# Optimization experiments

Hardware: AMD Instinct MI355X
Metric: run time of the kernel (lower is better)

## Reference

```python
import jax, jax.numpy as jnp
import numpy as np

NUM_SEGMENTS = 100000  # number of cycle slots (max cycle id + 1)


def setup_inputs() -> dict:
    key = jax.random.key(0)
    k1, k2, k3 = jax.random.split(key, 3)
    x = jax.random.randint(k1, (100000,), 0, 22, dtype=jnp.int64)
    atom_to_cycle = jax.random.randint(k2, (2, 600000), 0, NUM_SEGMENTS, dtype=jnp.int64)
    emb_weight = jax.random.normal(k3, (22, 128), dtype=jnp.float32)  # Embedding(22, hidden_dim)
    return {"x": x, "atom_to_cycle": atom_to_cycle, "emb_weight": emb_weight}


def reference(x, atom_to_cycle, emb_weight):
    # x: [N] int atom codes; atom_to_cycle: [2, E]; emb_weight: [22, D]
    h = emb_weight[x]                       # [N, D] embedding lookup
    gathered = h[atom_to_cycle[0]]          # [E, D] gather by atom index
    # scatter_sum over cycle ids -> [NUM_SEGMENTS, D]
    out = jax.ops.segment_sum(gathered, atom_to_cycle[1], num_segments=NUM_SEGMENTS)
    return out
```

## Files before the change

### kernel.cpp

```cpp
#include <hip/hip_runtime.h>
#include <stdint.h>

#define KCODES 22
#define KW     12

typedef int   int2v   __attribute__((ext_vector_type(2)));
typedef int   int4v   __attribute__((ext_vector_type(4)));
typedef float float4v __attribute__((ext_vector_type(4)));

#define BSHIFT   7
#define BROWS    128
#define BCAP     4096
#define EPT      8
#define CHUNK    2048
#define MAXBUCK  1024
#define GPAD     16

__global__ __launch_bounds__(256) void bin_edges(
        const int* __restrict__ a2c, const int* __restrict__ x,
        uint32_t* __restrict__ gcur, uint16_t* __restrict__ bins,
        int E, int nbuck) {
    __shared__ uint32_t lcnt[MAXBUCK];
    __shared__ uint32_t lbase[MAXBUCK];
    const int tid = threadIdx.x;
    for (int b = tid; b < nbuck; b += 256) lcnt[b] = 0;
    __syncthreads();

    const int base = blockIdx.x * CHUNK + tid * EPT;
    int atoms[EPT] __attribute__((aligned(16)));
    int cycs[EPT]  __attribute__((aligned(16)));
    if (((E & 3) == 0) && (base + EPT <= E)) {
        *(int4v*)(atoms + 0) = __builtin_nontemporal_load((const int4v*)(a2c + base));
        *(int4v*)(atoms + 4) = __builtin_nontemporal_load((const int4v*)(a2c + base) + 1);
        *(int4v*)(cycs + 0)  = __builtin_nontemporal_load((const int4v*)(a2c + E + base));
        *(int4v*)(cycs + 4)  = __builtin_nontemporal_load((const int4v*)(a2c + E + base) + 1);
    } else {
#pragma unroll
        for (int j = 0; j < EPT; ++j) {
            int e = base + j;
            atoms[j] = (e < E) ? a2c[e] : 0;
            cycs[j]  = (e < E) ? a2c[E + e] : -1;
        }
    }

    uint16_t val[EPT], bk[EPT], rk[EPT];
#pragma unroll
    for (int j = 0; j < EPT; ++j) {
        if (cycs[j] >= 0) {
            uint32_t code = (uint32_t)x[atoms[j]];
            uint32_t b    = (uint32_t)cycs[j] >> BSHIFT;
            bk[j]  = (uint16_t)b;
            rk[j]  = (uint16_t)atomicAdd(&lcnt[b], 1u);
            val[j] = (uint16_t)((((uint32_t)cycs[j] & (BROWS - 1)) << 5) | code);
        } else {
            bk[j] = 0xFFFFu;
        }
    }
    __syncthreads();

    for (int b = tid; b < nbuck; b += 256) {
        uint32_t c = lcnt[b];
        lbase[b] = c ? atomicAdd(&gcur[(size_t)b * GPAD], c) : 0u;
    }
    __syncthreads();

#pragma unroll
    for (int j = 0; j < EPT; ++j) {
        if (bk[j] != 0xFFFFu) {
            uint32_t idx = lbase[bk[j]] + rk[j];
            if (idx < BCAP)
                bins[(size_t)bk[j] * BCAP + idx] = val[j];
        }
    }
}

__global__ __launch_bounds__(256) void hist_expand(
        const uint32_t* __restrict__ gcur, const uint16_t* __restrict__ bins,
        const float* __restrict__ emb, float* __restrict__ out, int num_seg) {
    __shared__ uint32_t hist[BROWS * KW];
    const int tid = threadIdx.x;
    const int b   = blockIdx.x;
    const int d4  = tid & 31;
    const int sub = tid >> 5;

    float4v e[KCODES];
#pragma unroll
    for (int k = 0; k < KCODES; ++k)
        e[k] = ((const float4v*)emb)[k * 32 + d4];

    for (int i = tid; i < BROWS * KW; i += 256) hist[i] = 0;
    __syncthreads();

    int n = gcur[(size_t)b * GPAD]; if (n > BCAP) n = BCAP;
    const uint16_t* bb = bins + (size_t)b * BCAP;
    for (int i = tid; i < n; i += 256) {
        uint32_t v = bb[i];
        atomicAdd(&hist[(v >> 5) * KW + ((v & 31u) >> 1)], 1u << ((v & 1u) << 4));
    }
    __syncthreads();

    for (int r = sub; r < BROWS; r += 8) {
        int cyc = b * BROWS + r;
        if (cyc >= num_seg) break;
        const uint4* hrow = (const uint4*)&hist[r * KW];
        uint4 w0 = hrow[0], w1 = hrow[1], w2 = hrow[2];
        uint32_t wv[12] = {w0.x, w0.y, w0.z, w0.w,
                           w1.x, w1.y, w1.z, w1.w,
                           w2.x, w2.y, w2.z, w2.w};
        float4v acc = (float4v)(0.f);
#pragma unroll
        for (int w = 0; w < 11; ++w) {
            float c0 = (float)(wv[w] & 0xFFFFu);
            float c1 = (float)(wv[w] >> 16);
            float4v e0 = e[2 * w], e1 = e[2 * w + 1];
            acc.x = fmaf(c1, e1.x, fmaf(c0, e0.x, acc.x));
            acc.y = fmaf(c1, e1.y, fmaf(c0, e0.y, acc.y));
            acc.z = fmaf(c1, e1.z, fmaf(c0, e0.z, acc.z));
            acc.w = fmaf(c1, e1.w, fmaf(c0, e0.w, acc.w));
        }
        ((float4v*)out)[(size_t)cyc * 32 + d4] = acc;
    }
}

__global__ void count_edges2(const int* __restrict__ a2c,
                             const int* __restrict__ x,
                             uint32_t* __restrict__ cnt, int E) {
    int i = blockIdx.x * blockDim.x + threadIdx.x;
    int E2 = E >> 1;
    if (i < E2) {
        int2v a = __builtin_nontemporal_load(&((const int2v*)a2c)[i]);
        int2v c = __builtin_nontemporal_load(&((const int2v*)(a2c + E))[i]);
        uint32_t k0 = (uint32_t)x[a.x];
        uint32_t k1 = (uint32_t)x[a.y];
        atomicAdd(&cnt[(size_t)c.x * KW + (k0 >> 1)], 1u << ((k0 & 1) << 4));
        atomicAdd(&cnt[(size_t)c.y * KW + (k1 >> 1)], 1u << ((k1 & 1) << 4));
    }
}

__global__ void count_edges1(const int* __restrict__ a2c,
                             const int* __restrict__ x,
                             uint32_t* __restrict__ cnt, int E) {
    int e = blockIdx.x * blockDim.x + threadIdx.x;
    if (e < E) {
        int atom = a2c[e];
        int cyc  = a2c[E + e];
        uint32_t code = (uint32_t)x[atom];
        atomicAdd(&cnt[(size_t)cyc * KW + (code >> 1)], 1u << ((code & 1) << 4));
    }
}

__global__ __launch_bounds__(256) void expand_out(
        const uint32_t* __restrict__ cnt,
        const float* __restrict__ emb,
        float* __restrict__ out, int num_seg) {
    const int d4  = threadIdx.x & 31;
    const int sub = threadIdx.x >> 5;

    float4v e[KCODES];
#pragma unroll
    for (int k = 0; k < KCODES; ++k)
        e[k] = ((const float4v*)emb)[k * 32 + d4];

    for (int c = blockIdx.x * 8 + sub; c < num_seg; c += gridDim.x * 8) {
        const uint4* crow = (const uint4*)(cnt + (size_t)c * KW);
        uint4 w0 = crow[0], w1 = crow[1], w2 = crow[2];
        uint32_t wv[12] = {w0.x, w0.y, w0.z, w0.w,
                           w1.x, w1.y, w1.z, w1.w,
                           w2.x, w2.y, w2.z, w2.w};
        float4v acc = (float4v)(0.f);
#pragma unroll
        for (int w = 0; w < 11; ++w) {
            float c0 = (float)(wv[w] & 0xFFFFu);
            float c1 = (float)(wv[w] >> 16);
            float4v e0 = e[2 * w], e1 = e[2 * w + 1];
            acc.x = fmaf(c1, e1.x, fmaf(c0, e0.x, acc.x));
            acc.y = fmaf(c1, e1.y, fmaf(c0, e0.y, acc.y));
            acc.z = fmaf(c1, e1.z, fmaf(c0, e0.z, acc.z));
            acc.w = fmaf(c1, e1.w, fmaf(c0, e0.w, acc.w));
        }
        ((float4v*)out)[(size_t)c * 32 + d4] = acc;
    }
}

__global__ void zero_out_f4(float4* __restrict__ out, int n4) {
    int i = blockIdx.x * blockDim.x + threadIdx.x;
    if (i < n4) out[i] = make_float4(0.f, 0.f, 0.f, 0.f);
}

__global__ void scatter_edges(const int* __restrict__ a2c,
                              const int* __restrict__ x,
                              const float* __restrict__ emb,
                              float* __restrict__ out, int E) {
    int t = blockIdx.x * blockDim.x + threadIdx.x;
    int e = t >> 5;
    int d = (t & 31) * 4;
    if (e < E) {
        int atom = a2c[e];
        int cyc  = a2c[E + e];
        int code = x[atom];
        const float4 ev = ((const float4*)emb)[code * 32 + (d >> 2)];
        float* o = out + (size_t)cyc * 128 + d;
        atomicAdd(o + 0, ev.x);
        atomicAdd(o + 1, ev.y);
        atomicAdd(o + 2, ev.z);
        atomicAdd(o + 3, ev.w);
    }
}

extern "C" void kernel_launch(void* const* d_in, const int* in_sizes, int n_in,
                              void* d_out, int out_size, void* d_ws, size_t ws_size,
                              hipStream_t stream) {
    const int*   x    = (const int*)d_in[0];
    const int*   a2c  = (const int*)d_in[1];
    const float* emb  = (const float*)d_in[2];
    float*       out  = (float*)d_out;

    const int E       = in_sizes[1] / 2;
    const int D       = in_sizes[2] / KCODES;
    const int num_seg = out_size / D;

    const int nbuck = (num_seg + BROWS - 1) >> BSHIFT;
    const size_t cur_bytes = (size_t)nbuck * GPAD * sizeof(uint32_t);
    const size_t bins_off  = (cur_bytes + 65535) & ~(size_t)65535;
    const size_t need_bin  = bins_off + (size_t)nbuck * BCAP * sizeof(uint16_t);
    const size_t need_cnt  = (size_t)num_seg * KW * sizeof(uint32_t);

    if (nbuck <= MAXBUCK && ws_size >= need_bin) {
        uint32_t* gcur = (uint32_t*)d_ws;
        uint16_t* bins = (uint16_t*)((char*)d_ws + bins_off);

        (void)hipMemsetAsync(gcur, 0, cur_bytes, stream);

        int blocks1 = (E + CHUNK - 1) / CHUNK;
        bin_edges<<<blocks1, 256, 0, stream>>>(a2c, x, gcur, bins, E, nbuck);
        hist_expand<<<nbuck, 256, 0, stream>>>(gcur, bins, emb, out, num_seg);
    } else if (ws_size >= need_cnt) {
        uint32_t* cnt = (uint32_t*)d_ws;
        (void)hipMemsetAsync(cnt, 0, need_cnt, stream);
        if ((E & 1) == 0) {
            int E2 = E >> 1;
            count_edges2<<<(E2 + 255) / 256, 256, 0, stream>>>(a2c, x, cnt, E);
        } else {
            count_edges1<<<(E + 255) / 256, 256, 0, stream>>>(a2c, x, cnt, E);
        }
        int blocks = (num_seg + 7) / 8;
        if (blocks > 1024) blocks = 1024;
        expand_out<<<blocks, 256, 0, stream>>>(cnt, emb, out, num_seg);
    } else {
        int n4 = out_size / 4;
        zero_out_f4<<<(n4 + 255) / 256, 256, 0, stream>>>((float4*)out, n4);
        long long threads = (long long)E * 32;
        int blocks = (int)((threads + 255) / 256);
        scatter_edges<<<blocks, 256, 0, stream>>>(a2c, x, emb, out, E);
    }
    (void)n_in; (void)D;
}
```

Before: 107.0 us.

## Fuse workspace zeroing, edge binning and histogram expand into one cooperative kernel

Replaces the memset plus two kernel launches with a single cooperative kernel of 512 blocks. Grid-wide syncs separate the phases: zeroing the bucket counters, binning edges into per-bucket lists, and building per-bucket histograms that are expanded into the output. The goal is to remove the launch and inter-kernel gaps and to load the embedding table into registers only once. The cost is grid-sync overhead and a fixed grid that processes the 782 buckets in two uneven rounds, which may reduce parallelism in the expand phase. The atomic-count fallback path is removed.

```diff
diff --git a/kernel.cpp b/kernel.cpp
--- a/kernel.cpp
+++ b/kernel.cpp
@@ -1,5 +1,8 @@
 #include <hip/hip_runtime.h>
+#include <hip/hip_cooperative_groups.h>
 #include <stdint.h>
+
+namespace cg = cooperative_groups;
 
 #define KCODES 22
 #define KW     12
@@ -15,6 +18,128 @@
 #define CHUNK    2048
 #define MAXBUCK  1024
 #define GPAD     16
+#define GRID_F   512
+
+__global__ __launch_bounds__(256) void fused_all(
+        const int* __restrict__ a2c, const int* __restrict__ x,
+        const float* __restrict__ emb, float* __restrict__ out,
+        uint32_t* __restrict__ gcur, uint16_t* __restrict__ bins,
+        int E, int num_seg, int nbuck) {
+    cg::grid_group grid = cg::this_grid();
+
+    __shared__ union {
+        struct { uint32_t lcnt[MAXBUCK]; uint32_t lbase[MAXBUCK]; } p1;
+        uint32_t hist[BROWS * KW];
+    } sh;
+
+    const int tid = threadIdx.x;
+    const int d4  = tid & 31;
+    const int sub = tid >> 5;
+
+    float4v e[KCODES];
+#pragma unroll
+    for (int k = 0; k < KCODES; ++k)
+        e[k] = ((const float4v*)emb)[k * 32 + d4];
+
+    const int gsz = (int)gridDim.x * 256;
+    for (int i = blockIdx.x * 256 + tid; i < nbuck * GPAD; i += gsz)
+        __hip_atomic_store(&gcur[i], 0u, __ATOMIC_RELAXED, __HIP_MEMORY_SCOPE_AGENT);
+    grid.sync();
+
+    const int nchunk = (E + CHUNK - 1) / CHUNK;
+    if (blockIdx.x < nchunk) {
+        for (int b = tid; b < nbuck; b += 256) sh.p1.lcnt[b] = 0;
+        __syncthreads();
+
+        const int base = blockIdx.x * CHUNK + tid * EPT;
+        int atoms[EPT] __attribute__((aligned(16)));
+        int cycs[EPT]  __attribute__((aligned(16)));
+        if (((E & 3) == 0) && (base + EPT <= E)) {
+            *(int4v*)(atoms + 0) = __builtin_nontemporal_load((const int4v*)(a2c + base));
+            *(int4v*)(atoms + 4) = __builtin_nontemporal_load((const int4v*)(a2c + base) + 1);
+            *(int4v*)(cycs + 0)  = __builtin_nontemporal_load((const int4v*)(a2c + E + base));
+            *(int4v*)(cycs + 4)  = __builtin_nontemporal_load((const int4v*)(a2c + E + base) + 1);
+        } else {
+#pragma unroll
+            for (int j = 0; j < EPT; ++j) {
+                int ei = base + j;
+                atoms[j] = (ei < E) ? a2c[ei] : 0;
+                cycs[j]  = (ei < E) ? a2c[E + ei] : -1;
+            }
+        }
+
+        uint16_t val[EPT], bk[EPT], rk[EPT];
+#pragma unroll
+        for (int j = 0; j < EPT; ++j) {
+            if (cycs[j] >= 0) {
+                uint32_t code = (uint32_t)x[atoms[j]];
+                uint32_t b    = (uint32_t)cycs[j] >> BSHIFT;
+                bk[j]  = (uint16_t)b;
+                rk[j]  = (uint16_t)atomicAdd(&sh.p1.lcnt[b], 1u);
+                val[j] = (uint16_t)((((uint32_t)cycs[j] & (BROWS - 1)) << 5) | code);
+            } else {
+                bk[j] = 0xFFFFu;
+            }
+        }
+        __syncthreads();
+
+        for (int b = tid; b < nbuck; b += 256) {
+            uint32_t c = sh.p1.lcnt[b];
+            sh.p1.lbase[b] = c ? atomicAdd(&gcur[(size_t)b * GPAD], c) : 0u;
+        }
+        __syncthreads();
+
+#pragma unroll
+        for (int j = 0; j < EPT; ++j) {
+            if (bk[j] != 0xFFFFu) {
+                uint32_t idx = sh.p1.lbase[bk[j]] + rk[j];
+                if (idx < BCAP)
+                    __hip_atomic_store(&bins[(size_t)bk[j] * BCAP + idx], val[j],
+                                       __ATOMIC_RELAXED, __HIP_MEMORY_SCOPE_AGENT);
+            }
+        }
+    }
+    grid.sync();
+
+    for (int b = blockIdx.x; b < nbuck; b += (int)gridDim.x) {
+        for (int i = tid; i < BROWS * KW; i += 256) sh.hist[i] = 0;
+        __syncthreads();
+
+        int n = (int)__hip_atomic_load(&gcur[(size_t)b * GPAD],
+                                       __ATOMIC_RELAXED, __HIP_MEMORY_SCOPE_AGENT);
+        if (n > BCAP) n = BCAP;
+        const uint16_t* bb = bins + (size_t)b * BCAP;
+        for (int i = tid; i < n; i += 256) {
+            uint32_t v = (uint32_t)__hip_atomic_load(&bb[i],
+                                       __ATOMIC_RELAXED, __HIP_MEMORY_SCOPE_AGENT);
+            atomicAdd(&sh.hist[(v >> 5) * KW + ((v & 31u) >> 1)], 1u << ((v & 1u) << 4));
+        }
+        __syncthreads();
+
+        for (int r = sub; r < BROWS; r += 8) {
+            int cyc = b * BROWS + r;
+            if (cyc >= num_seg) break;
+            const uint4* hrow = (const uint4*)&sh.hist[r * KW];
+            uint4 w0 = hrow[0], w1 = hrow[1], w2 = hrow[2];
+            uint32_t wv[12] = {w0.x, w0.y, w0.z, w0.w,
+                               w1.x, w1.y, w1.z, w1.w,
+                               w2.x, w2.y, w2.z, w2.w};
+            float4v acc = (float4v)(0.f);
+#pragma unroll
+            for (int w = 0; w < 11; ++w) {
+                float c0 = (float)(wv[w] & 0xFFFFu);
+                float c1 = (float)(wv[w] >> 16);
+                float4v e0 = e[2 * w], e1 = e[2 * w + 1];
+                acc.x = fmaf(c1, e1.x, fmaf(c0, e0.x, acc.x));
+                acc.y = fmaf(c1, e1.y, fmaf(c0, e0.y, acc.y));
+                acc.z = fmaf(c1, e1.z, fmaf(c0, e0.z, acc.z));
+                acc.w = fmaf(c1, e1.w, fmaf(c0, e0.w, acc.w));
+            }
+            ((float4v*)out)[(size_t)cyc * 32 + d4] = acc;
+        }
+        __syncthreads();
+    }
+}
 
 __global__ __launch_bounds__(256) void bin_edges(
         const int* __restrict__ a2c, const int* __restrict__ x,
@@ -119,66 +244,6 @@
             acc.w = fmaf(c1, e1.w, fmaf(c0, e0.w, acc.w));
         }
         ((float4v*)out)[(size_t)cyc * 32 + d4] = acc;
-    }
-}
-
-__global__ void count_edges2(const int* __restrict__ a2c,
-                             const int* __restrict__ x,
-                             uint32_t* __restrict__ cnt, int E) {
-    int i = blockIdx.x * blockDim.x + threadIdx.x;
-    int E2 = E >> 1;
-    if (i < E2) {
-        int2v a = __builtin_nontemporal_load(&((const int2v*)a2c)[i]);
-        int2v c = __builtin_nontemporal_load(&((const int2v*)(a2c + E))[i]);
-        uint32_t k0 = (uint32_t)x[a.x];
-        uint32_t k1 = (uint32_t)x[a.y];
-        atomicAdd(&cnt[(size_t)c.x * KW + (k0 >> 1)], 1u << ((k0 & 1) << 4));
-        atomicAdd(&cnt[(size_t)c.y * KW + (k1 >> 1)], 1u << ((k1 & 1) << 4));
-    }
-}
-
-__global__ void count_edges1(const int* __restrict__ a2c,
-                             const int* __restrict__ x,
-                             uint32_t* __restrict__ cnt, int E) {
-    int e = blockIdx.x * blockDim.x + threadIdx.x;
-    if (e < E) {
-        int atom = a2c[e];
-        int cyc  = a2c[E + e];
-        uint32_t code = (uint32_t)x[atom];
-        atomicAdd(&cnt[(size_t)cyc * KW + (code >> 1)], 1u << ((code & 1) << 4));
-    }
-}
-
-__global__ __launch_bounds__(256) void expand_out(
-        const uint32_t* __restrict__ cnt,
-        const float* __restrict__ emb,
-        float* __restrict__ out, int num_seg) {
-    const int d4  = threadIdx.x & 31;
-    const int sub = threadIdx.x >> 5;
-
-    float4v e[KCODES];
-#pragma unroll
-    for (int k = 0; k < KCODES; ++k)
-        e[k] = ((const float4v*)emb)[k * 32 + d4];
-
-    for (int c = blockIdx.x * 8 + sub; c < num_seg; c += gridDim.x * 8) {
-        const uint4* crow = (const uint4*)(cnt + (size_t)c * KW);
-        uint4 w0 = crow[0], w1 = crow[1], w2 = crow[2];
-        uint32_t wv[12] = {w0.x, w0.y, w0.z, w0.w,
-                           w1.x, w1.y, w1.z, w1.w,
-                           w2.x, w2.y, w2.z, w2.w};
-        float4v acc = (float4v)(0.f);
-#pragma unroll
-        for (int w = 0; w < 11; ++w) {
-            float c0 = (float)(wv[w] & 0xFFFFu);
-            float c1 = (float)(wv[w] >> 16);
-            float4v e0 = e[2 * w], e1 = e[2 * w + 1];
-            acc.x = fmaf(c1, e1.x, fmaf(c0, e0.x, acc.x));
-            acc.y = fmaf(c1, e1.y, fmaf(c0, e0.y, acc.y));
-            acc.z = fmaf(c1, e1.z, fmaf(c0, e0.z, acc.z));
-            acc.w = fmaf(c1, e1.w, fmaf(c0, e0.w, acc.w));
-        }
-        ((float4v*)out)[(size_t)c * 32 + d4] = acc;
     }
 }
 
@@ -229,23 +294,19 @@
         uint32_t* gcur = (uint32_t*)d_ws;
         uint16_t* bins = (uint16_t*)((char*)d_ws + bins_off);
 
-        (void)hipMemsetAsync(gcur, 0, cur_bytes, stream);
-
-        int blocks1 = (E + CHUNK - 1) / CHUNK;
-        bin_edges<<<blocks1, 256, 0, stream>>>(a2c, x, gcur, bins, E, nbuck);
-        hist_expand<<<nbuck, 256, 0, stream>>>(gcur, bins, emb, out, num_seg);
-    } else if (ws_size >= need_cnt) {
-        uint32_t* cnt = (uint32_t*)d_ws;
-        (void)hipMemsetAsync(cnt, 0, need_cnt, stream);
-        if ((E & 1) == 0) {
-            int E2 = E >> 1;
-            count_edges2<<<(E2 + 255) / 256, 256, 0, stream>>>(a2c, x, cnt, E);
-        } else {
-            count_edges1<<<(E + 255) / 256, 256, 0, stream>>>(a2c, x, cnt, E);
-        }
-        int blocks = (num_seg + 7) / 8;
-        if (blocks > 1024) blocks = 1024;
-        expand_out<<<blocks, 256, 0, stream>>>(cnt, emb, out, num_seg);
+        int E_ = E, ns_ = num_seg, nb_ = nbuck;
+        const int* a2c_ = a2c; const int* x_ = x; const float* emb_ = emb; float* out_ = out;
+        uint32_t* gcur_ = gcur; uint16_t* bins_ = bins;
+        void* args[] = {&a2c_, &x_, &emb_, &out_, &gcur_, &bins_, &E_, &ns_, &nb_};
+        hipError_t err = hipLaunchCooperativeKernel((const void*)fused_all,
+                                                    dim3(GRID_F), dim3(256),
+                                                    args, 0, stream);
+        if (err != hipSuccess) {
+            (void)hipMemsetAsync(gcur, 0, cur_bytes, stream);
+            int blocks1 = (E + CHUNK - 1) / CHUNK;
+            bin_edges<<<blocks1, 256, 0, stream>>>(a2c, x, gcur, bins, E, nbuck);
+            hist_expand<<<nbuck, 256, 0, stream>>>(gcur, bins, emb, out, num_seg);
+        }
     } else {
         int n4 = out_size / 4;
         zero_out_f4<<<(n4 + 255) / 256, 256, 0, stream>>>((float4*)out, n4);
@@ -253,5 +314,5 @@
         int blocks = (int)((threads + 255) / 256);
         scatter_edges<<<blocks, 256, 0, stream>>>(a2c, x, emb, out, E);
     }
-    (void)n_in; (void)D;
-}
+    (void)n_in; (void)D; (void)need_cnt;
+}
```

After: 235.0 us. 2.2x slower.
